# Optimization experiments

Hardware: AMD Instinct MI355X
Metric: run time of the kernel (lower is better)

The kernel has to match this reference:

```python
import jax, jax.numpy as jnp
import numpy as np

H = 256          # hidden_dim
OD = 1           # out_dim
N_PTS = 262144   # number of points in the graph
PATCH_ID = 995   # hard-coded patch index in the original forward
MNK = 10         # bins per axis (M = N = K = 10)


def _mlp(h, layers):
    # Linear/Tanh chain, no activation after the last Linear (matches nn.Sequential)
    for w, b in layers[:-1]:
        h = jnp.tanh(h @ w + b)
    w, b = layers[-1]
    return h @ w + b


def _patch_idx(x):
    # Vectorized replacement of the per-point Python binning loop:
    # floor(coord * 10), clamp to [0, 9], flatten to patch id, select PATCH_ID.
    c = np.clip(np.floor(np.asarray(x) * float(MNK)).astype(np.int64), 0, MNK - 1)
    pid = c[:, 0] * (MNK * MNK) + c[:, 1] * MNK + c[:, 2]
    return np.nonzero(pid == PATCH_ID)[0]


def setup_inputs() -> dict:
    key = jax.random.key(0)
    ks = iter(jax.random.split(key, 40))
    d = {}
    d["x"] = jax.random.uniform(next(ks), (N_PTS, 3), jnp.float32)   # coords in [0,1)
    d["y"] = jax.random.normal(next(ks), (N_PTS, OD), jnp.float32)

    def add(prefix, dims):
        for i, (fi, fo) in enumerate(dims):
            bound = 1.0 / np.sqrt(fi)  # PyTorch Linear default init
            d[f"{prefix}_w{i}"] = jax.random.uniform(next(ks), (fi, fo), jnp.float32, -bound, bound)
            d[f"{prefix}_b{i}"] = jax.random.uniform(next(ks), (fo,), jnp.float32, -bound, bound)

    branch_dims = [(3, H), (H, H), (H, H), (H, OD * H)]
    add("tb", branch_dims)   # total_branch
    add("br", branch_dims)   # branchs[0]
    add("tr", branch_dims)   # trunks[0]
    add("o", [(3 * H, H), (H, H), (H, OD)])  # outs[0]
    return d


def reference(x, y,
              tb_w0, tb_b0, tb_w1, tb_b1, tb_w2, tb_b2, tb_w3, tb_b3,
              br_w0, br_b0, br_w1, br_b1, br_w2, br_b2, br_w3, br_b3,
              tr_w0, tr_b0, tr_w1, tr_b1, tr_w2, tr_b2, tr_w3, tr_b3,
              o_w0, o_b0, o_w1, o_b1, o_w2, o_b2):
    idx = jnp.asarray(_patch_idx(x))  # points that fall into patch 995

    tb = [(tb_w0, tb_b0), (tb_w1, tb_b1), (tb_w2, tb_b2), (tb_w3, tb_b3)]
    br = [(br_w0, br_b0), (br_w1, br_b1), (br_w2, br_b2), (br_w3, br_b3)]
    tr = [(tr_w0, tr_b0), (tr_w1, tr_b1), (tr_w2, tr_b2), (tr_w3, tr_b3)]
    o = [(o_w0, o_b0), (o_w1, o_b1), (o_w2, o_b2)]

    global_param = jnp.max(_mlp(x, tb), axis=0)  # (OD*H,)  = amax over points
    local_param = jnp.max(_mlp(x, br), axis=0)   # (OD*H,)

    x_patch = x[idx]                              # (MM, 3)
    gt_patch = y[idx]                             # (MM, OD)

    local_coord = _mlp(x_patch, tr)               # (MM, OD*H)
    MM = local_coord.shape[0]
    feat = jnp.concatenate([
        local_coord,
        jnp.broadcast_to(local_param, (MM, local_param.shape[0])),
        jnp.broadcast_to(global_param, (MM, global_param.shape[0])),
    ], axis=-1)                                   # (MM, 3*H) since OD=1
    pred_patch = _mlp(feat, o)                    # (MM, OD)
    return pred_patch, gt_patch
```

## Files before the change

kernel.cpp:

```cpp
#include <hip/hip_runtime.h>

typedef __bf16 bf16x8 __attribute__((ext_vector_type(8)));
typedef float f32x4 __attribute__((ext_vector_type(4)));

#define WT_SLOT 65536
#define WS_GKEYS 0
#define WS_VEC0  4096
#define WS_COUNTS 8192
#define WS_BASES 12288
#define WS_IDX   16384
#define WS_WT    32768

#define TANH_K 2.8853900817779268f

__device__ __forceinline__ unsigned fkey(float f) {
  unsigned u = __float_as_uint(f);
  return (u & 0x80000000u) ? ~u : (u | 0x80000000u);
}
__device__ __forceinline__ float unfkey(unsigned k) {
  unsigned u = (k & 0x80000000u) ? (k & 0x7FFFFFFFu) : ~k;
  return __uint_as_float(u);
}
__device__ __forceinline__ int lds_off(int r, int cb) {
  return r * 512 + (cb ^ ((r & 7) << 4));
}
__device__ __forceinline__ float tanh_scaled(float t) {
  float e = __builtin_amdgcn_exp2f(t);
  return fmaf(__builtin_amdgcn_rcpf(e + 1.0f), -2.0f, 1.0f);
}
__device__ __forceinline__ unsigned cvt_pk_bf16(float lo, float hi) {
  unsigned d;
  asm("v_cvt_pk_bf16_f32 %0, %1, %2" : "=v"(d) : "v"(lo), "v"(hi));
  return d;
}

__device__ __forceinline__ void load_bpair(const __bf16* wt, int wave, int lane, int p,
                                           bf16x8 b[8]) {
  const __bf16* base = wt + p * 16384 + wave * 2048 + lane * 8;
#pragma unroll
  for (int h = 0; h < 2; ++h)
#pragma unroll
    for (int i = 0; i < 4; ++i)
      b[h * 4 + i] = *(const bf16x8*)(base + h * 8192 + i * 512);
}

__device__ __forceinline__ void compute_pair(char* lds, const bf16x8 bc[8], int ksbase,
                                             int rlo, int khi2, f32x4 acc[8][4]) {
#pragma unroll
  for (int h = 0; h < 2; ++h) {
    int cb = (ksbase + h) * 64 + khi2;
#pragma unroll
    for (int rt = 0; rt < 8; ++rt) {
      bf16x8 av = *(const bf16x8*)(lds + lds_off(rt * 16 + rlo, cb));
#pragma unroll
      for (int i = 0; i < 4; ++i)
        acc[rt][i] = __builtin_amdgcn_mfma_f32_16x16x32_bf16(bc[h * 4 + i], av, acc[rt][i], 0, 0, 0);
    }
  }
}

template <bool TANH, bool WRITE, bool CMAX>
__device__ __forceinline__ void epilogue(char* lds, int lane, int wave,
                                         f32x4 acc[8][4], float* mbuf) {
  const int rlo = lane & 15;
  const int q4 = (lane >> 4) << 2;
#pragma unroll
  for (int i = 0; i < 4; ++i) {
    const int cbase = (wave * 4 + i) * 16 + q4;
    f32x4 cm;
#pragma unroll
    for (int rt = 0; rt < 8; ++rt) {
      f32x4 v;
#pragma unroll
      for (int rg = 0; rg < 4; ++rg) {
        float t = acc[rt][i][rg];
        if (TANH) t = tanh_scaled(t);
        v[rg] = t;
      }
      if (WRITE) {
        uint2 pv;
        pv.x = cvt_pk_bf16(v[0], v[1]);
        pv.y = cvt_pk_bf16(v[2], v[3]);
        *(uint2*)(lds + lds_off(rt * 16 + rlo, 2 * cbase)) = pv;
      }
      if (CMAX) {
        if (rt == 0) cm = v;
        else {
#pragma unroll
          for (int rg = 0; rg < 4; ++rg) cm[rg] = fmaxf(cm[rg], v[rg]);
        }
      }
    }
    if (CMAX) {
#pragma unroll
      for (int rg = 0; rg < 4; ++rg) {
#pragma unroll
        for (int off = 1; off <= 8; off <<= 1)
          cm[rg] = fmaxf(cm[rg], __shfl_xor(cm[rg], off, 64));
      }
      if (rlo == 0) *(f32x4*)(mbuf + cbase) = cm;
    }
  }
}

template <bool TANH>
__device__ __forceinline__ void acc_init(f32x4 acc[8][4], const float* bias, int lane, int wave) {
  const int q4 = (lane >> 4) << 2;
#pragma unroll
  for (int i = 0; i < 4; ++i) {
    f32x4 bv = *(const f32x4*)(bias + (wave * 4 + i) * 16 + q4);
    if (TANH) {
#pragma unroll
      for (int rg = 0; rg < 4; ++rg) bv[rg] *= TANH_K;
    }
#pragma unroll
    for (int rt = 0; rt < 8; ++rt) acc[rt][i] = bv;
  }
}

template <bool TANH, bool WRITE, bool CMAX>
__device__ __forceinline__ void layer256(char* lds, const __bf16* wt, const __bf16* wt_next,
                                         const float* bias, int lane, int wave, float* mbuf,
                                         bf16x8 b0[8], bf16x8 b1[8]) {
  const int rlo = lane & 15;
  const int khi2 = (lane >> 4) << 4;
  f32x4 acc[8][4];
  acc_init<TANH>(acc, bias, lane, wave);

  load_bpair(wt, wave, lane, 1, b1);
  compute_pair(lds, b0, 0, rlo, khi2, acc);
  load_bpair(wt, wave, lane, 2, b0);
  compute_pair(lds, b1, 2, rlo, khi2, acc);
  load_bpair(wt, wave, lane, 3, b1);
  compute_pair(lds, b0, 4, rlo, khi2, acc);
  load_bpair(wt_next, wave, lane, 0, b0);
  compute_pair(lds, b1, 6, rlo, khi2, acc);

  __syncthreads();
  epilogue<TANH, WRITE, CMAX>(lds, lane, wave, acc, mbuf);
  __syncthreads();
}

__device__ __forceinline__ void layer0_mfma(char* lds, const char* mini, const bf16x8 b0f[4],
                                            const float* bias, int lane, int wave) {
  const int rlo = lane & 15;
  const int khi2 = (lane >> 4) << 4;
  f32x4 acc[8][4];
  acc_init<true>(acc, bias, lane, wave);
#pragma unroll
  for (int rt = 0; rt < 8; ++rt) {
    bf16x8 av = *(const bf16x8*)(mini + (rt * 16 + rlo) * 64 + khi2);
#pragma unroll
    for (int i = 0; i < 4; ++i)
      acc[rt][i] = __builtin_amdgcn_mfma_f32_16x16x32_bf16(b0f[i], av, acc[rt][i], 0, 0, 0);
  }
  epilogue<true, true, false>(lds, lane, wave, acc, nullptr);
  __syncthreads();
}

struct ConvArgs { const float* src[14]; };
__global__ void K_conv(ConvArgs a, __bf16* wt, unsigned* gkeys) {
  int job = blockIdx.x, t = threadIdx.x, y = blockIdx.y;
  if (job == 14) {
    if (y == 0) { gkeys[t] = 0u; gkeys[256 + t] = 0u; }
    return;
  }
  if (job >= 11) {
    if (y >= 2) return;
    const float* s = a.src[job];
    __bf16* d = wt + (size_t)11 * WT_SLOT + (job - 11) * 8192;
#pragma unroll
    for (int it = 0; it < 16; ++it) {
      int p = y * 4096 + it * 256 + t;
      int nt = (p >> 9) & 15, ln = (p >> 3) & 63, j = p & 7;
      int n = nt * 16 + (ln & 15);
      int k = ((ln >> 4) << 3) + j;
      d[p] = (k < 3) ? (__bf16)(TANH_K * s[k * 256 + n]) : (__bf16)0.f;
    }
    return;
  }
  const float scale = (job >= 9 || (job % 3) != 2) ? TANH_K : 1.0f;
  const float* s = a.src[job];
  __bf16* d = wt + (size_t)job * WT_SLOT;
#pragma unroll
  for (int it = 0; it < 16; ++it) {
    int p = y * 4096 + it * 256 + t;
    int ks = p >> 13, nt = (p >> 9) & 15, ln = (p >> 3) & 63, j = p & 7;
    int n = nt * 16 + (ln & 15);
    int k = ks * 32 + ((ln >> 4) << 3) + j;
    d[p] = (__bf16)(scale * s[(k << 8) | n]);
  }
}

struct BigArgs {
  const float* x;
  const __bf16* wt;
  const float* b0[2]; const float* b1[2]; const float* b2[2]; const float* b3[2];
  unsigned* gkeys;
};
__global__ __launch_bounds__(256, 2) void K_big(BigArgs a) {
  __shared__ char lds[73728];
  int tid = threadIdx.x, lane = tid & 63, wave = tid >> 6;
  int mlp = blockIdx.x >> 11;
  int row0 = (blockIdx.x & 2047) << 7;
  const __bf16* wt = a.wt + (size_t)(mlp * 3) * WT_SLOT;
  const __bf16* w0f = a.wt + (size_t)11 * WT_SLOT + mlp * 8192;
  char* mini = lds + 65536;
  {
    const float* xr = a.x + (size_t)row0 * 3;
    for (int s = tid; s < 512; s += 256) {
      int r = s & 127, ch = s >> 7;
      bf16x8 v;
#pragma unroll
      for (int j = 0; j < 8; ++j) v[j] = (__bf16)0.f;
      if (ch == 0) {
        v[0] = (__bf16)xr[r * 3]; v[1] = (__bf16)xr[r * 3 + 1]; v[2] = (__bf16)xr[r * 3 + 2];
      }
      *(bf16x8*)(mini + r * 64 + ch * 16) = v;
    }
  }
  bf16x8 b0f[4];
#pragma unroll
  for (int i = 0; i < 4; ++i) b0f[i] = *(const bf16x8*)(w0f + (wave * 4 + i) * 512 + lane * 8);
  bf16x8 br0[8], br1[8];
  load_bpair(wt, wave, lane, 0, br0);
  __syncthreads();
  layer0_mfma(lds, mini, b0f, a.b0[mlp], lane, wave);
  float* mbuf = (float*)mini;
  layer256<true, true, false>(lds, wt, wt + WT_SLOT, a.b1[mlp], lane, wave, nullptr, br0, br1);
  layer256<true, true, false>(lds, wt + WT_SLOT, wt + 2 * WT_SLOT, a.b2[mlp], lane, wave, nullptr, br0, br1);
  layer256<false, false, true>(lds, wt + 2 * WT_SLOT, wt + 2 * WT_SLOT, a.b3[mlp], lane, wave, mbuf, br0, br1);
  atomicMax(a.gkeys + mlp * 256 + tid, fkey(mbuf[tid]));
}

__device__ __forceinline__ bool in_patch(const float* x, int r) {
  float a = x[r * 3], b = x[r * 3 + 1], c = x[r * 3 + 2];
  int c0 = min(max((int)floorf(a * 10.0f), 0), 9);
  int c1 = min(max((int)floorf(b * 10.0f), 0), 9);
  int c2 = min(max((int)floorf(c * 10.0f), 0), 9);
  return (c0 == 9) && (c1 == 9) && (c2 == 5);
}
__global__ void K_count(const float* x, unsigned* counts) {
  __shared__ unsigned sw[4];
  int b = blockIdx.x, t = threadIdx.x;
  int base = b * 1024 + t * 4;
  unsigned c = 0;
#pragma unroll
  for (int j = 0; j < 4; ++j) c += in_patch(x, base + j) ? 1u : 0u;
#pragma unroll
  for (int o = 1; o < 64; o <<= 1) c += __shfl_xor((int)c, o, 64);
  if ((t & 63) == 0) sw[t >> 6] = c;
  __syncthreads();
  if (t == 0) counts[b] = sw[0] + sw[1] + sw[2] + sw[3];
}
__global__ void K_scan(const unsigned* counts, unsigned* bases) {
  __shared__ unsigned s[256];
  int t = threadIdx.x;
  unsigned c = counts[t];
  s[t] = c; __syncthreads();
  for (int o = 1; o < 256; o <<= 1) {
    unsigned v = (t >= o) ? s[t - o] : 0u;
    __syncthreads();
    s[t] += v;
    __syncthreads();
  }
  bases[t] = s[t] - c;
}
__global__ void K_fill(const float* x, const unsigned* bases, int* idx) {
  __shared__ unsigned s[256];
  int b = blockIdx.x, t = threadIdx.x;
  int base = b * 1024 + t * 4;
  unsigned fm = 0, c = 0;
#pragma unroll
  for (int j = 0; j < 4; ++j) {
    bool f = in_patch(x, base + j);
    fm |= (f ? 1u : 0u) << j;
    c += f ? 1u : 0u;
  }
  s[t] = c; __syncthreads();
  for (int o = 1; o < 256; o <<= 1) {
    unsigned v = (t >= o) ? s[t - o] : 0u;
    __syncthreads();
    s[t] += v;
    __syncthreads();
  }
  unsigned pos = bases[b] + s[t] - c;
#pragma unroll
  for (int j = 0; j < 4; ++j)
    if (fm & (1u << j)) idx[pos++] = base + j;
}

__global__ void K_vec(const unsigned* gkeys, const float* ow0, const float* ob0, float* vec0) {
  __shared__ float gp[256], lp[256];
  int t = threadIdx.x;
  gp[t] = unfkey(gkeys[t]);
  lp[t] = unfkey(gkeys[256 + t]);
  __syncthreads();
  float acc = ob0[t];
  for (int k = 0; k < 256; ++k) {
    acc = fmaf(lp[k], ow0[(256 + k) * 256 + t], acc);
    acc = fmaf(gp[k], ow0[(512 + k) * 256 + t], acc);
  }
  vec0[t] = acc;
}

struct SmallArgs {
  const float* x; const float* y; const int* idx; int MM;
  const __bf16* wt;
  const float* trb0; const float* trb1; const float* trb2; const float* trb3;
  const float* vec0; const float* ob1; const float* ow2; const float* ob2;
  float* out;
};
__global__ __launch_bounds__(256, 2) void K_small(SmallArgs a) {
  __shared__ char lds[73728];
  int tid = threadIdx.x, lane = tid & 63, wave = tid >> 6;
  int pr0 = blockIdx.x << 7;
  const __bf16* wt6 = a.wt + (size_t)6 * WT_SLOT;
  const __bf16* w0f = a.wt + (size_t)11 * WT_SLOT + 2 * 8192;
  char* mini = lds + 65536;
  {
    for (int s = tid; s < 512; s += 256) {
      int r = s & 127, ch = s >> 7;
      bf16x8 v;
#pragma unroll
      for (int j = 0; j < 8; ++j) v[j] = (__bf16)0.f;
      if (ch == 0) {
        int j = a.idx[min(pr0 + r, a.MM - 1)];
        v[0] = (__bf16)a.x[j * 3]; v[1] = (__bf16)a.x[j * 3 + 1]; v[2] = (__bf16)a.x[j * 3 + 2];
      }
      *(bf16x8*)(mini + r * 64 + ch * 16) = v;
    }
  }
  if (tid < 128 && pr0 + tid < a.MM) a.out[a.MM + pr0 + tid] = a.y[a.idx[pr0 + tid]];
  bf16x8 b0f[4];
#pragma unroll
  for (int i = 0; i < 4; ++i) b0f[i] = *(const bf16x8*)(w0f + (wave * 4 + i) * 512 + lane * 8);
  bf16x8 br0[8], br1[8];
  load_bpair(wt6, wave, lane, 0, br0);
  __syncthreads();
  layer0_mfma(lds, mini, b0f, a.trb0, lane, wave);
  layer256<true, true, false>(lds, wt6, wt6 + WT_SLOT, a.trb1, lane, wave, nullptr, br0, br1);
  layer256<true, true, false>(lds, wt6 + WT_SLOT, wt6 + 2 * WT_SLOT, a.trb2, lane, wave, nullptr, br0, br1);
  layer256<false, true, false>(lds, wt6 + 2 * WT_SLOT, a.wt + (size_t)9 * WT_SLOT, a.trb3, lane, wave, nullptr, br0, br1);
  layer256<true, true, false>(lds, a.wt + (size_t)9 * WT_SLOT, a.wt + (size_t)10 * WT_SLOT, a.vec0, lane, wave, nullptr, br0, br1);
  layer256<true, true, false>(lds, a.wt + (size_t)10 * WT_SLOT, a.wt + (size_t)10 * WT_SLOT, a.ob1, lane, wave, nullptr, br0, br1);
  {
    int r = tid >> 1, half = tid & 1, pr = pr0 + r;
    float s = 0.f;
    for (int i = 0; i < 128; ++i) {
      int c = (half << 7) + i;
      s = fmaf((float)*(const __bf16*)(lds + lds_off(r, 2 * c)), a.ow2[c], s);
    }
    s += __shfl_xor(s, 1, 64);
    if (half == 0 && pr < a.MM) a.out[pr] = s + a.ob2[0];
  }
}

extern "C" void kernel_launch(void* const* d_in, const int* in_sizes, int n_in,
                              void* d_out, int out_size, void* d_ws, size_t ws_size,
                              hipStream_t stream) {
  const float* x = (const float*)d_in[0];
  const float* y = (const float*)d_in[1];
  char* ws = (char*)d_ws;
  unsigned* gkeys = (unsigned*)(ws + WS_GKEYS);
  float* vec0 = (float*)(ws + WS_VEC0);
  unsigned* counts = (unsigned*)(ws + WS_COUNTS);
  unsigned* bases = (unsigned*)(ws + WS_BASES);
  int* idx = (int*)(ws + WS_IDX);
  __bf16* wt = (__bf16*)(ws + WS_WT);
  int MM = out_size / 2;

  ConvArgs ca;
  for (int m = 0; m < 3; ++m)
    for (int L = 0; L < 3; ++L)
      ca.src[m * 3 + L] = (const float*)d_in[2 + m * 8 + 2 * (L + 1)];
  ca.src[9] = (const float*)d_in[26];
  ca.src[10] = (const float*)d_in[28];
  ca.src[11] = (const float*)d_in[2];
  ca.src[12] = (const float*)d_in[10];
  ca.src[13] = (const float*)d_in[18];
  hipLaunchKernelGGL(K_conv, dim3(15, 16), dim3(256), 0, stream, ca, wt, gkeys);

  K_count<<<256, 256, 0, stream>>>(x, counts);
  K_scan<<<1, 256, 0, stream>>>(counts, bases);
  K_fill<<<256, 256, 0, stream>>>(x, bases, idx);

  BigArgs ba;
  ba.x = x; ba.wt = wt; ba.gkeys = gkeys;
  ba.b0[0] = (const float*)d_in[3];  ba.b1[0] = (const float*)d_in[5];
  ba.b2[0] = (const float*)d_in[7];  ba.b3[0] = (const float*)d_in[9];
  ba.b0[1] = (const float*)d_in[11]; ba.b1[1] = (const float*)d_in[13];
  ba.b2[1] = (const float*)d_in[15]; ba.b3[1] = (const float*)d_in[17];
  K_big<<<4096, 256, 0, stream>>>(ba);

  K_vec<<<1, 256, 0, stream>>>(gkeys, (const float*)d_in[26], (const float*)d_in[27], vec0);

  if (MM > 0) {
    SmallArgs sa;
    sa.x = x; sa.y = y; sa.idx = idx; sa.MM = MM; sa.wt = wt;
    sa.trb0 = (const float*)d_in[19]; sa.trb1 = (const float*)d_in[21];
    sa.trb2 = (const float*)d_in[23]; sa.trb3 = (const float*)d_in[25];
    sa.vec0 = vec0;
    sa.ob1 = (const float*)d_in[29];
    sa.ow2 = (const float*)d_in[30]; sa.ob2 = (const float*)d_in[31];
    sa.out = (float*)d_out;
    K_small<<<(MM + 127) / 128, 256, 0, stream>>>(sa);
  }
}
```

Measured before the change: 254.7 us.

## Load layer-0 inputs into registers and widen LDS swizzle to sixteen rows

Layer-0 input fragments now go straight from global memory into per-lane registers instead of being staged through a small LDS buffer, which removes the staging writes and one block barrier. K_small's LDS allocation drops to 64 KiB. K_big also shrinks its main buffer to 64 KiB but adds a separate 1 KiB max buffer, so its total LDS barely changes. The LDS XOR swizzle now uses the low 4 row bits instead of 3, aiming to cut bank conflicts on the 512-byte row stride. The register fragments raise VGPR pressure early in the kernel, and the mbuf aliasing changes, so correctness depends on the epilogue indexing still matching.

```diff
diff --git a/kernel.cpp b/kernel.cpp
--- a/kernel.cpp
+++ b/kernel.cpp
@@ -22,7 +22,7 @@
   return __uint_as_float(u);
 }
 __device__ __forceinline__ int lds_off(int r, int cb) {
-  return r * 512 + (cb ^ ((r & 7) << 4));
+  return r * 512 + (cb ^ ((r & 15) << 4));
 }
 __device__ __forceinline__ float tanh_scaled(float t) {
   float e = __builtin_amdgcn_exp2f(t);
@@ -141,18 +141,15 @@
   __syncthreads();
 }
 
-__device__ __forceinline__ void layer0_mfma(char* lds, const char* mini, const bf16x8 b0f[4],
+__device__ __forceinline__ void layer0_mfma(char* lds, const bf16x8 av[8], const bf16x8 b0f[4],
                                             const float* bias, int lane, int wave) {
-  const int rlo = lane & 15;
-  const int khi2 = (lane >> 4) << 4;
   f32x4 acc[8][4];
   acc_init<true>(acc, bias, lane, wave);
 #pragma unroll
   for (int rt = 0; rt < 8; ++rt) {
-    bf16x8 av = *(const bf16x8*)(mini + (rt * 16 + rlo) * 64 + khi2);
 #pragma unroll
     for (int i = 0; i < 4; ++i)
-      acc[rt][i] = __builtin_amdgcn_mfma_f32_16x16x32_bf16(b0f[i], av, acc[rt][i], 0, 0, 0);
+      acc[rt][i] = __builtin_amdgcn_mfma_f32_16x16x32_bf16(b0f[i], av[rt], acc[rt][i], 0, 0, 0);
   }
   epilogue<true, true, false>(lds, lane, wave, acc, nullptr);
   __syncthreads();
@@ -199,24 +196,27 @@
   unsigned* gkeys;
 };
 __global__ __launch_bounds__(256, 2) void K_big(BigArgs a) {
-  __shared__ char lds[73728];
+  __shared__ char lds[65536];
+  __shared__ float mbuf[256];
   int tid = threadIdx.x, lane = tid & 63, wave = tid >> 6;
   int mlp = blockIdx.x >> 11;
   int row0 = (blockIdx.x & 2047) << 7;
   const __bf16* wt = a.wt + (size_t)(mlp * 3) * WT_SLOT;
   const __bf16* w0f = a.wt + (size_t)11 * WT_SLOT + mlp * 8192;
-  char* mini = lds + 65536;
+  const int rlo = lane & 15;
+  bf16x8 av[8];
   {
     const float* xr = a.x + (size_t)row0 * 3;
-    for (int s = tid; s < 512; s += 256) {
-      int r = s & 127, ch = s >> 7;
+#pragma unroll
+    for (int rt = 0; rt < 8; ++rt) {
       bf16x8 v;
 #pragma unroll
       for (int j = 0; j < 8; ++j) v[j] = (__bf16)0.f;
-      if (ch == 0) {
-        v[0] = (__bf16)xr[r * 3]; v[1] = (__bf16)xr[r * 3 + 1]; v[2] = (__bf16)xr[r * 3 + 2];
-      }
-      *(bf16x8*)(mini + r * 64 + ch * 16) = v;
+      if (lane < 16) {
+        const float* p = xr + (rt * 16 + rlo) * 3;
+        v[0] = (__bf16)p[0]; v[1] = (__bf16)p[1]; v[2] = (__bf16)p[2];
+      }
+      av[rt] = v;
     }
   }
   bf16x8 b0f[4];
@@ -224,9 +224,7 @@
   for (int i = 0; i < 4; ++i) b0f[i] = *(const bf16x8*)(w0f + (wave * 4 + i) * 512 + lane * 8);
   bf16x8 br0[8], br1[8];
   load_bpair(wt, wave, lane, 0, br0);
-  __syncthreads();
-  layer0_mfma(lds, mini, b0f, a.b0[mlp], lane, wave);
-  float* mbuf = (float*)mini;
+  layer0_mfma(lds, av, b0f, a.b0[mlp], lane, wave);
   layer256<true, true, false>(lds, wt, wt + WT_SLOT, a.b1[mlp], lane, wave, nullptr, br0, br1);
   layer256<true, true, false>(lds, wt + WT_SLOT, wt + 2 * WT_SLOT, a.b2[mlp], lane, wave, nullptr, br0, br1);
   layer256<false, false, true>(lds, wt + 2 * WT_SLOT, wt + 2 * WT_SLOT, a.b3[mlp], lane, wave, mbuf, br0, br1);
@@ -312,23 +310,24 @@
   float* out;
 };
 __global__ __launch_bounds__(256, 2) void K_small(SmallArgs a) {
-  __shared__ char lds[73728];
+  __shared__ char lds[65536];
   int tid = threadIdx.x, lane = tid & 63, wave = tid >> 6;
   int pr0 = blockIdx.x << 7;
   const __bf16* wt6 = a.wt + (size_t)6 * WT_SLOT;
   const __bf16* w0f = a.wt + (size_t)11 * WT_SLOT + 2 * 8192;
-  char* mini = lds + 65536;
+  const int rlo = lane & 15;
+  bf16x8 av[8];
   {
-    for (int s = tid; s < 512; s += 256) {
-      int r = s & 127, ch = s >> 7;
+#pragma unroll
+    for (int rt = 0; rt < 8; ++rt) {
       bf16x8 v;
 #pragma unroll
       for (int j = 0; j < 8; ++j) v[j] = (__bf16)0.f;
-      if (ch == 0) {
-        int j = a.idx[min(pr0 + r, a.MM - 1)];
+      if (lane < 16) {
+        int j = a.idx[min(pr0 + rt * 16 + rlo, a.MM - 1)];
         v[0] = (__bf16)a.x[j * 3]; v[1] = (__bf16)a.x[j * 3 + 1]; v[2] = (__bf16)a.x[j * 3 + 2];
       }
-      *(bf16x8*)(mini + r * 64 + ch * 16) = v;
+      av[rt] = v;
     }
   }
   if (tid < 128 && pr0 + tid < a.MM) a.out[a.MM + pr0 + tid] = a.y[a.idx[pr0 + tid]];
@@ -337,8 +336,7 @@
   for (int i = 0; i < 4; ++i) b0f[i] = *(const bf16x8*)(w0f + (wave * 4 + i) * 512 + lane * 8);
   bf16x8 br0[8], br1[8];
   load_bpair(wt6, wave, lane, 0, br0);
-  __syncthreads();
-  layer0_mfma(lds, mini, b0f, a.trb0, lane, wave);
+  layer0_mfma(lds, av, b0f, a.trb0, lane, wave);
   layer256<true, true, false>(lds, wt6, wt6 + WT_SLOT, a.trb1, lane, wave, nullptr, br0, br1);
   layer256<true, true, false>(lds, wt6 + WT_SLOT, wt6 + 2 * WT_SLOT, a.trb2, lane, wave, nullptr, br0, br1);
   layer256<false, true, false>(lds, wt6 + 2 * WT_SLOT, a.wt + (size_t)9 * WT_SLOT, a.trb3, lane, wave, nullptr, br0, br1);
```

Result: no change. 259.2 us (+1.8%).
